# Kernel optimization log

Hardware: AMD Instinct MI355X
Metric: run time of the kernel (lower is better)

## Reference

```python
import jax, jax.numpy as jnp
import numpy as np

B, L, E, D = 4, 4096, 768, 64

def setup_inputs() -> dict:
    key = jax.random.key(0)
    ks = jax.random.split(key, 7)
    x = jax.random.normal(ks[0], (B, L, E), dtype=jnp.float32)
    # True = masked (strict upper triangle), as in masked_fill semantics
    causal_mask = jnp.triu(jnp.ones((L, L), dtype=bool), k=1)
    # True = valid token (inverted with ~ inside forward); all valid to avoid NaN rows
    pad_mask = jnp.ones((B, L), dtype=bool)
    s = 1.0 / np.sqrt(E)
    Wk = jax.random.uniform(ks[1], (E, D), jnp.float32, -s, s)
    bk = jax.random.uniform(ks[2], (D,), jnp.float32, -s, s)
    Wq = jax.random.uniform(ks[3], (E, D), jnp.float32, -s, s)
    bq = jax.random.uniform(ks[4], (D,), jnp.float32, -s, s)
    Wv = jax.random.uniform(ks[5], (E, D), jnp.float32, -s, s)
    bv = jax.random.uniform(ks[6], (D,), jnp.float32, -s, s)
    return {"x": x, "causal_mask": causal_mask, "pad_mask": pad_mask,
            "Wk": Wk, "bk": bk, "Wq": Wq, "bq": bq, "Wv": Wv, "bv": bv}

def reference(x, causal_mask, pad_mask, Wk, bk, Wq, bq, Wv, bv):
    # Linear projections: [B,L,E] @ [E,D] + [D]
    K = jnp.einsum('ble,ed->bld', x, Wk) + bk
    Q = jnp.einsum('ble,ed->bld', x, Wq) + bq
    V = jnp.einsum('ble,ed->bld', x, Wv) + bv
    d = Q.shape[-1]
    scores = jnp.einsum('bqd,bkd->bqk', Q, K) / jnp.sqrt(jnp.asarray(d, Q.dtype))
    # full_mask: causal (True=masked) OR key-position padding (~pad_mask, broadcast over query dim)
    full_mask = causal_mask[None, :, :] | (~pad_mask)[:, None, :]
    scores = jnp.where(full_mask, -jnp.inf, scores)
    attn = jax.nn.softmax(scores, axis=-1)
    out = jnp.einsum('bqk,bkd->bqd', attn, V)
    return out
```

## Files before the change

### kernel.cpp

```cpp
#include <hip/hip_runtime.h>

#define L_SEQ 4096
#define BATCH 4
#define EDIM 768

typedef __attribute__((ext_vector_type(8))) short bf16x8;
typedef __attribute__((ext_vector_type(4))) float f32x4;
typedef __attribute__((ext_vector_type(16))) float f32x16;
typedef __attribute__((ext_vector_type(4))) unsigned short u16x4;
typedef __attribute__((ext_vector_type(8))) unsigned short u16x8;
typedef __attribute__((ext_vector_type(2))) _Float16 f16x2;
typedef __attribute__((ext_vector_type(4))) _Float16 f16x4;

__device__ __forceinline__ unsigned short f2bf(float f) {
  unsigned u = __builtin_bit_cast(unsigned, f);
  u += 0x7FFFu + ((u >> 16) & 1u);
  return (unsigned short)(u >> 16);
}

__device__ __forceinline__ f16x4 half_of(u16x8 v, int h) {
  u16x4 t = h ? (u16x4){v[4], v[5], v[6], v[7]} : (u16x4){v[0], v[1], v[2], v[3]};
  return __builtin_bit_cast(f16x4, t);
}

__device__ __forceinline__ f16x2 pkrtz(float a, float b) {
  return __builtin_bit_cast(f16x2, __builtin_amdgcn_cvt_pkrtz(a, b));
}

__global__ __launch_bounds__(256) void prep_kernel(
    const float* __restrict__ Wq, const float* __restrict__ Wk,
    const float* __restrict__ Wv, unsigned short* __restrict__ WT) {
  int g = blockIdx.x * 256 + threadIdx.x;
  if (g >= 192 * EDIM) return;
  int row = g / EDIM, k = g - row * EDIM;
  int z = row >> 6, n = row & 63;
  const float* W = (z == 0) ? Wq : (z == 1) ? Wk : Wv;
  WT[g] = f2bf(W[k * 64 + n]);
}

__global__ __launch_bounds__(256) void proj_kernel(
    const float* __restrict__ x, const unsigned short* __restrict__ WT,
    const float* __restrict__ bq, const float* __restrict__ bk, const float* __restrict__ bv,
    unsigned short* __restrict__ Qf, unsigned short* __restrict__ Kf,
    unsigned short* __restrict__ Vf) {
  __shared__ unsigned short SH[2 * 13824];
  int tid = threadIdx.x;
  int w = tid >> 6, lane = tid & 63, l15 = lane & 15, g4 = lane >> 4;
  int m0 = blockIdx.x * 64;
  int brow = tid >> 3, bsg = tid & 7;

  f32x4 acc[3][4];
#pragma unroll
  for (int z = 0; z < 3; z++)
#pragma unroll
    for (int cf = 0; cf < 4; cf++) acc[z][cf] = (f32x4){0.f, 0.f, 0.f, 0.f};

  f32x4 arA[4], arB[4];
  u16x8 brA[6], brB[6];

  auto loadA = [&](f32x4 (&ar)[4], int k0) {
    const float* xp = x + (size_t)(m0 + 16 * w + l15) * EDIM + k0 + g4 * 8;
    ar[0] = *(const f32x4*)xp;
    ar[1] = *(const f32x4*)(xp + 4);
    ar[2] = *(const f32x4*)(xp + 32);
    ar[3] = *(const f32x4*)(xp + 36);
  };
  auto loadB = [&](u16x8 (&br)[6], int k0) {
#pragma unroll
    for (int pp = 0; pp < 6; pp++)
      br[pp] = *(const u16x8*)(WT + (size_t)(brow + pp * 32) * EDIM + k0 + bsg * 8);
  };
  auto writeB = [&](int cur, u16x8 (&br)[6]) {
#pragma unroll
    for (int pp = 0; pp < 6; pp++)
      *(u16x8*)&SH[cur * 13824 + (brow + pp * 32) * 72 + bsg * 8] = br[pp];
  };
  auto mkfrag = [&](f32x4 lo, f32x4 hi) {
    union { u16x8 u; bf16x8 b; } r;
    r.u[0] = f2bf(lo[0]); r.u[1] = f2bf(lo[1]); r.u[2] = f2bf(lo[2]); r.u[3] = f2bf(lo[3]);
    r.u[4] = f2bf(hi[0]); r.u[5] = f2bf(hi[1]); r.u[6] = f2bf(hi[2]); r.u[7] = f2bf(hi[3]);
    return r.b;
  };
  auto compute = [&](int cur, f32x4 (&ar)[4]) {
#pragma unroll
    for (int ks = 0; ks < 2; ks++) {
      bf16x8 a = mkfrag(ar[ks * 2], ar[ks * 2 + 1]);
#pragma unroll
      for (int z = 0; z < 3; z++)
#pragma unroll
        for (int cf = 0; cf < 4; cf++) {
          bf16x8 bb = *(const bf16x8*)&SH[cur * 13824 + (z * 64 + cf * 16 + l15) * 72 +
                                          ks * 32 + g4 * 8];
          acc[z][cf] = __builtin_amdgcn_mfma_f32_16x16x32_bf16(a, bb, acc[z][cf], 0, 0, 0);
        }
    }
  };

  loadA(arA, 0);
  loadB(brA, 0);
  for (int ss = 0; ss < 6; ss++) {
    int k1 = (2 * ss + 1) * 64;
    loadA(arB, k1);
    loadB(brB, k1);
    writeB(0, brA);
    __syncthreads();
    compute(0, arA);
    if (ss < 5) {
      int k2 = (2 * ss + 2) * 64;
      loadA(arA, k2);
      loadB(brA, k2);
    }
    writeB(1, brB);
    __syncthreads();
    compute(1, arB);
  }

  __syncthreads();
  unsigned short* LQ = SH;
  unsigned short* LK = SH + 4096;
  unsigned short* LV = SH + 8192;
#pragma unroll
  for (int cf = 0; cf < 4; cf++) {
    int d = cf * 16 + l15;
    float bqv = bq[d], bkv = bk[d], bvv = bv[d];
#pragma unroll
    for (int r = 0; r < 4; r++) {
      int t = 16 * w + g4 * 4 + r;
      int sl = t >> 5, tl = t & 31;
      int fqk = sl * 2048 + (d >> 4) * 512 + (tl + ((d >> 3) & 1) * 32) * 8 + (d & 7);
      LQ[fqk] = f2bf((acc[0][cf][r] + bqv) * 0.125f);
      LK[fqk] = f2bf(acc[1][cf][r] + bkv);
      int fv = sl * 2048 + (d >> 5) * 1024 + ((tl >> 4) & 1) * 512 +
               ((d & 31) + ((tl >> 2) & 1) * 32) * 8 + ((tl >> 3) & 1) * 4 + (tl & 3);
      _Float16 hv = (_Float16)(acc[2][cf][r] + bvv);
      LV[fv] = __builtin_bit_cast(unsigned short, hv);
    }
  }
  __syncthreads();
  {
    int bb = m0 >> 12;
    int S0 = (m0 >> 5) & 127;
    size_t base = ((size_t)(bb * 128 + S0)) * 2048;
    u16x8* dq = (u16x8*)(Qf + base);
    u16x8* dk = (u16x8*)(Kf + base);
    u16x8* dv = (u16x8*)(Vf + base);
    const u16x8* sq = (const u16x8*)LQ;
    const u16x8* sk = (const u16x8*)LK;
    const u16x8* sv = (const u16x8*)LV;
    dq[tid * 2] = sq[tid * 2]; dq[tid * 2 + 1] = sq[tid * 2 + 1];
    dk[tid * 2] = sk[tid * 2]; dk[tid * 2 + 1] = sk[tid * 2 + 1];
    dv[tid * 2] = sv[tid * 2]; dv[tid * 2 + 1] = sv[tid * 2 + 1];
  }
}

__global__ __launch_bounds__(512, 2) void attn_kernel(
    const unsigned short* __restrict__ Qf, const unsigned short* __restrict__ Kf,
    const unsigned short* __restrict__ Vf, float* __restrict__ out) {
  __shared__ float OB[8][32][68];
  __shared__ float ML[8][2][32];
  int tid = threadIdx.x;
  int w = tid >> 6, lane = tid & 63;
  int ql = lane & 31, hi = lane >> 5;
  int blk = blockIdx.x;
  int xcd = blk & 7;
  int b = xcd >> 1;
  int pid = ((xcd & 1) << 5) | (blk >> 3);
  int sA = pid, sB = 127 - pid;
  size_t bL = (size_t)b * L_SEQ;
  const unsigned short* Qb = Qf + (size_t)b * 128 * 2048;
  const unsigned short* Kb = Kf + (size_t)b * 128 * 2048;
  const unsigned short* Vb = Vf + (size_t)b * 128 * 2048;

  bf16x8 qA[4], qB[4];
#pragma unroll
  for (int kh = 0; kh < 4; kh++) {
    qA[kh] = *(const bf16x8*)(Qb + ((size_t)sA * 4 + kh) * 512 + lane * 8);
    qB[kh] = *(const bf16x8*)(Qb + ((size_t)sB * 4 + kh) * 512 + lane * 8);
  }
  f32x16 oA0, oA1, oB0, oB1;
#pragma unroll
  for (int i = 0; i < 16; i++) { oA0[i] = 0.f; oA1[i] = 0.f; oB0[i] = 0.f; oB1[i] = 0.f; }
  float mA = -1e38f, lA = 0.f, mB = -1e38f, lB = 0.f;

  auto loadKV = [&](bf16x8 (&kf)[4], u16x8 (&vf)[4], int j) {
    const unsigned short* kp = Kb + (size_t)j * 2048 + lane * 8;
    const unsigned short* vp = Vb + (size_t)j * 2048 + lane * 8;
#pragma unroll
    for (int q = 0; q < 4; q++) kf[q] = *(const bf16x8*)(kp + q * 512);
#pragma unroll
    for (int q = 0; q < 4; q++) vf[q] = *(const u16x8*)(vp + q * 512);
  };

  auto strip = [&](bf16x8 (&kf)[4], u16x8 (&vf)[4], int j, int s, bf16x8 (&qf)[4],
                   f32x16& o0, f32x16& o1, float& m, float& l) {
    f32x16 st;
#pragma unroll
    for (int i = 0; i < 16; i++) st[i] = 0.f;
    __builtin_amdgcn_s_setprio(1);
#pragma unroll
    for (int kh = 0; kh < 4; kh++)
      st = __builtin_amdgcn_mfma_f32_32x32x16_bf16(kf[kh], qf[kh], st, 0, 0, 0);
    __builtin_amdgcn_s_setprio(0);

    if (j == s) {
#pragma unroll
      for (int r = 0; r < 16; r++) {
        int tl = (r & 3) + 8 * (r >> 2) + 4 * hi;
        if (tl > ql) st[r] = -1e30f;
      }
    }

    float mx = st[0];
#pragma unroll
    for (int r = 1; r < 16; r++) mx = fmaxf(mx, st[r]);
    mx = fmaxf(mx, __shfl_xor(mx, 32));
    if (!__all(mx <= m + 8.0f)) {
      float mn = fmaxf(m, mx);
      float sc = __expf(m - mn);
      m = mn; l *= sc;
#pragma unroll
      for (int i = 0; i < 16; i++) { o0[i] *= sc; o1[i] *= sc; }
    }
    float rs = 0.f;
#pragma unroll
    for (int r = 0; r < 16; r++) { st[r] = __expf(st[r] - m); rs += st[r]; }
    rs += __shfl_xor(rs, 32);
    l += rs;

    f16x4 pb[4];
#pragma unroll
    for (int oc = 0; oc < 4; oc++) {
      f16x2 a = pkrtz(st[4 * oc], st[4 * oc + 1]);
      f16x2 c = pkrtz(st[4 * oc + 2], st[4 * oc + 3]);
      pb[oc] = (f16x4){a[0], a[1], c[0], c[1]};
    }
    __builtin_amdgcn_s_setprio(1);
#pragma unroll
    for (int oc = 0; oc < 4; oc++)
      o0 = __builtin_amdgcn_mfma_f32_32x32x8f16(half_of(vf[oc >> 1], oc & 1), pb[oc], o0, 0, 0, 0);
#pragma unroll
    for (int oc = 0; oc < 4; oc++)
      o1 = __builtin_amdgcn_mfma_f32_32x32x8f16(half_of(vf[2 + (oc >> 1)], oc & 1), pb[oc], o1, 0, 0, 0);
    __builtin_amdgcn_s_setprio(0);
  };

  auto step = [&](bf16x8 (&kf)[4], u16x8 (&vf)[4], int j) {
    if (j <= sA) strip(kf, vf, j, sA, qA, oA0, oA1, mA, lA);
    strip(kf, vf, j, sB, qB, oB0, oB1, mB, lB);
  };

  bf16x8 kfA[4], kfB[4];
  u16x8 vfA[4], vfB[4];
  {
    int j = w;
    loadKV(kfA, vfA, j);
    while (true) {
      int jn = j + 8;
      bool hasB = (jn <= sB);
      if (hasB) loadKV(kfB, vfB, jn);
      step(kfA, vfA, j);
      if (!hasB) break;
      j = jn;
      jn = j + 8;
      bool hasA = (jn <= sB);
      if (hasA) loadKV(kfA, vfA, jn);
      step(kfB, vfB, j);
      if (!hasA) break;
      j = jn;
    }
  }

  auto stash_reduce = [&](int s, f32x16& o0, f32x16& o1, float m, float l) {
    __syncthreads();
#pragma unroll
    for (int g = 0; g < 4; g++) {
      *(f32x4*)&OB[w][ql][8 * g + 4 * hi] =
          (f32x4){o0[4 * g], o0[4 * g + 1], o0[4 * g + 2], o0[4 * g + 3]};
      *(f32x4*)&OB[w][ql][32 + 8 * g + 4 * hi] =
          (f32x4){o1[4 * g], o1[4 * g + 1], o1[4 * g + 2], o1[4 * g + 3]};
    }
    if (hi == 0) { ML[w][0][ql] = m; ML[w][1][ql] = l; }
    __syncthreads();
    int q = tid >> 4, dg = tid & 15;
    float mw[8], lw[8];
    float ms = -1e38f;
#pragma unroll
    for (int ww = 0; ww < 8; ww++) {
      mw[ww] = ML[ww][0][q]; lw[ww] = ML[ww][1][q];
      ms = fmaxf(ms, mw[ww]);
    }
    float denom = 0.f, ew[8];
#pragma unroll
    for (int ww = 0; ww < 8; ww++) { ew[ww] = __expf(mw[ww] - ms); denom += lw[ww] * ew[ww]; }
    float inv = 1.0f / denom;
    f32x4 acc = (f32x4){0.f, 0.f, 0.f, 0.f};
#pragma unroll
    for (int ww = 0; ww < 8; ww++) {
      f32x4 v = *(const f32x4*)&OB[ww][q][dg * 4];
      acc += v * ew[ww];
    }
    acc *= inv;
    *(f32x4*)(out + (bL + (size_t)s * 32 + q) * 64 + dg * 4) = acc;
  };
  stash_reduce(sA, oA0, oA1, mA, lA);
  stash_reduce(sB, oB0, oB1, mB, lB);
}

extern "C" void kernel_launch(void* const* d_in, const int* in_sizes, int n_in,
                              void* d_out, int out_size, void* d_ws, size_t ws_size,
                              hipStream_t stream) {
  const float* x  = (const float*)d_in[0];
  const float* Wk = (const float*)d_in[3];
  const float* bk = (const float*)d_in[4];
  const float* Wq = (const float*)d_in[5];
  const float* bq = (const float*)d_in[6];
  const float* Wv = (const float*)d_in[7];
  const float* bv = (const float*)d_in[8];
  float* out = (float*)d_out;

  char* ws = (char*)d_ws;
  unsigned short* WT = (unsigned short*)ws;
  unsigned short* Qf = (unsigned short*)(ws + 294912);
  unsigned short* Kf = (unsigned short*)(ws + 294912 + 2097152);
  unsigned short* Vf = (unsigned short*)(ws + 294912 + 2 * 2097152);

  prep_kernel<<<576, 256, 0, stream>>>(Wq, Wk, Wv, WT);
  proj_kernel<<<256, 256, 0, stream>>>(x, WT, bq, bk, bv, Qf, Kf, Vf);
  attn_kernel<<<256, 512, 0, stream>>>(Qf, Kf, Vf, out);
}
```

Before: 48.13 us.

## Split projection into smaller tiles, use exp2 softmax, stagger K/V loads

The projection kernel now computes 32 rows per block across 512 blocks. Its four waves split as two row halves by two column halves, so each wave covers 96 output columns instead of all 192. The attention kernel folds log2(e) into the Q scale and uses exp2f in place of __expf, widening the lazy-rescale threshold to match. It also issues the next K loads and V loads separately, interleaved between the two strips. Together these aim to raise projection parallelism, cut exponent instruction cost, and spread memory traffic, at the cost of reloading the weight tiles in more blocks.

After: 53.98 us. 1.12x slower.

```diff
diff --git a/kernel.cpp b/kernel.cpp
--- a/kernel.cpp
+++ b/kernel.cpp
@@ -11,6 +11,8 @@
 typedef __attribute__((ext_vector_type(8))) unsigned short u16x8;
 typedef __attribute__((ext_vector_type(2))) _Float16 f16x2;
 typedef __attribute__((ext_vector_type(4))) _Float16 f16x4;
+
+#define QSCALE (0.125f * 1.4426950408889634f)
 
 __device__ __forceinline__ unsigned short f2bf(float f) {
   unsigned u = __builtin_bit_cast(unsigned, f);
@@ -46,20 +48,19 @@
   __shared__ unsigned short SH[2 * 13824];
   int tid = threadIdx.x;
   int w = tid >> 6, lane = tid & 63, l15 = lane & 15, g4 = lane >> 4;
-  int m0 = blockIdx.x * 64;
+  int rw = w & 1, ch = w >> 1;
+  int m0 = blockIdx.x * 32;
   int brow = tid >> 3, bsg = tid & 7;
 
-  f32x4 acc[3][4];
-#pragma unroll
-  for (int z = 0; z < 3; z++)
-#pragma unroll
-    for (int cf = 0; cf < 4; cf++) acc[z][cf] = (f32x4){0.f, 0.f, 0.f, 0.f};
+  f32x4 acc[6];
+#pragma unroll
+  for (int cf = 0; cf < 6; cf++) acc[cf] = (f32x4){0.f, 0.f, 0.f, 0.f};
 
   f32x4 arA[4], arB[4];
   u16x8 brA[6], brB[6];
 
   auto loadA = [&](f32x4 (&ar)[4], int k0) {
-    const float* xp = x + (size_t)(m0 + 16 * w + l15) * EDIM + k0 + g4 * 8;
+    const float* xp = x + (size_t)(m0 + 16 * rw + l15) * EDIM + k0 + g4 * 8;
     ar[0] = *(const f32x4*)xp;
     ar[1] = *(const f32x4*)(xp + 4);
     ar[2] = *(const f32x4*)(xp + 32);
@@ -86,13 +87,11 @@
     for (int ks = 0; ks < 2; ks++) {
       bf16x8 a = mkfrag(ar[ks * 2], ar[ks * 2 + 1]);
 #pragma unroll
-      for (int z = 0; z < 3; z++)
-#pragma unroll
-        for (int cf = 0; cf < 4; cf++) {
-          bf16x8 bb = *(const bf16x8*)&SH[cur * 13824 + (z * 64 + cf * 16 + l15) * 72 +
-                                          ks * 32 + g4 * 8];
-          acc[z][cf] = __builtin_amdgcn_mfma_f32_16x16x32_bf16(a, bb, acc[z][cf], 0, 0, 0);
-        }
+      for (int cf = 0; cf < 6; cf++) {
+        bf16x8 bb = *(const bf16x8*)&SH[cur * 13824 + (ch * 96 + cf * 16 + l15) * 72 +
+                                        ks * 32 + g4 * 8];
+        acc[cf] = __builtin_amdgcn_mfma_f32_16x16x32_bf16(a, bb, acc[cf], 0, 0, 0);
+      }
     }
   };
 
@@ -117,39 +116,37 @@
 
   __syncthreads();
   unsigned short* LQ = SH;
-  unsigned short* LK = SH + 4096;
-  unsigned short* LV = SH + 8192;
-#pragma unroll
-  for (int cf = 0; cf < 4; cf++) {
-    int d = cf * 16 + l15;
-    float bqv = bq[d], bkv = bk[d], bvv = bv[d];
+  unsigned short* LK = SH + 2048;
+  unsigned short* LV = SH + 4096;
+#pragma unroll
+  for (int cf = 0; cf < 6; cf++) {
+    int c = ch * 96 + cf * 16 + l15;
+    int z = c >> 6, d = c & 63;
+    float bb_ = (z == 0) ? bq[d] : (z == 1) ? bk[d] : bv[d];
 #pragma unroll
     for (int r = 0; r < 4; r++) {
-      int t = 16 * w + g4 * 4 + r;
-      int sl = t >> 5, tl = t & 31;
-      int fqk = sl * 2048 + (d >> 4) * 512 + (tl + ((d >> 3) & 1) * 32) * 8 + (d & 7);
-      LQ[fqk] = f2bf((acc[0][cf][r] + bqv) * 0.125f);
-      LK[fqk] = f2bf(acc[1][cf][r] + bkv);
-      int fv = sl * 2048 + (d >> 5) * 1024 + ((tl >> 4) & 1) * 512 +
-               ((d & 31) + ((tl >> 2) & 1) * 32) * 8 + ((tl >> 3) & 1) * 4 + (tl & 3);
-      _Float16 hv = (_Float16)(acc[2][cf][r] + bvv);
-      LV[fv] = __builtin_bit_cast(unsigned short, hv);
+      int tl = rw * 16 + g4 * 4 + r;
+      float v = acc[cf][r] + bb_;
+      if (z == 2) {
+        int fv = (d >> 5) * 1024 + ((tl >> 4) & 1) * 512 +
+                 ((d & 31) + ((tl >> 2) & 1) * 32) * 8 + ((tl >> 3) & 1) * 4 + (tl & 3);
+        _Float16 hv = (_Float16)v;
+        LV[fv] = __builtin_bit_cast(unsigned short, hv);
+      } else {
+        int fqk = (d >> 4) * 512 + (tl + ((d >> 3) & 1) * 32) * 8 + (d & 7);
+        if (z == 0) LQ[fqk] = f2bf(v * QSCALE);
+        else        LK[fqk] = f2bf(v);
+      }
     }
   }
   __syncthreads();
   {
-    int bb = m0 >> 12;
+    int b_ = m0 >> 12;
     int S0 = (m0 >> 5) & 127;
-    size_t base = ((size_t)(bb * 128 + S0)) * 2048;
-    u16x8* dq = (u16x8*)(Qf + base);
-    u16x8* dk = (u16x8*)(Kf + base);
-    u16x8* dv = (u16x8*)(Vf + base);
-    const u16x8* sq = (const u16x8*)LQ;
-    const u16x8* sk = (const u16x8*)LK;
-    const u16x8* sv = (const u16x8*)LV;
-    dq[tid * 2] = sq[tid * 2]; dq[tid * 2 + 1] = sq[tid * 2 + 1];
-    dk[tid * 2] = sk[tid * 2]; dk[tid * 2 + 1] = sk[tid * 2 + 1];
-    dv[tid * 2] = sv[tid * 2]; dv[tid * 2 + 1] = sv[tid * 2 + 1];
+    size_t base = ((size_t)(b_ * 128 + S0)) * 2048;
+    ((u16x8*)(Qf + base))[tid] = ((const u16x8*)LQ)[tid];
+    ((u16x8*)(Kf + base))[tid] = ((const u16x8*)LK)[tid];
+    ((u16x8*)(Vf + base))[tid] = ((const u16x8*)LV)[tid];
   }
 }
 
@@ -182,11 +179,13 @@
   for (int i = 0; i < 16; i++) { oA0[i] = 0.f; oA1[i] = 0.f; oB0[i] = 0.f; oB1[i] = 0.f; }
   float mA = -1e38f, lA = 0.f, mB = -1e38f, lB = 0.f;
 
-  auto loadKV = [&](bf16x8 (&kf)[4], u16x8 (&vf)[4], int j) {
+  auto loadK = [&](bf16x8 (&kf)[4], int j) {
     const unsigned short* kp = Kb + (size_t)j * 2048 + lane * 8;
+#pragma unroll
+    for (int q = 0; q < 4; q++) kf[q] = *(const bf16x8*)(kp + q * 512);
+  };
+  auto loadV = [&](u16x8 (&vf)[4], int j) {
     const unsigned short* vp = Vb + (size_t)j * 2048 + lane * 8;
-#pragma unroll
-    for (int q = 0; q < 4; q++) kf[q] = *(const bf16x8*)(kp + q * 512);
 #pragma unroll
     for (int q = 0; q < 4; q++) vf[q] = *(const u16x8*)(vp + q * 512);
   };
@@ -214,16 +213,16 @@
 #pragma unroll
     for (int r = 1; r < 16; r++) mx = fmaxf(mx, st[r]);
     mx = fmaxf(mx, __shfl_xor(mx, 32));
-    if (!__all(mx <= m + 8.0f)) {
+    if (!__all(mx <= m + 11.0f)) {
       float mn = fmaxf(m, mx);
-      float sc = __expf(m - mn);
+      float sc = exp2f(m - mn);
       m = mn; l *= sc;
 #pragma unroll
       for (int i = 0; i < 16; i++) { o0[i] *= sc; o1[i] *= sc; }
     }
     float rs = 0.f;
 #pragma unroll
-    for (int r = 0; r < 16; r++) { st[r] = __expf(st[r] - m); rs += st[r]; }
+    for (int r = 0; r < 16; r++) { st[r] = exp2f(st[r] - m); rs += st[r]; }
     rs += __shfl_xor(rs, 32);
     l += rs;
 
@@ -244,27 +243,27 @@
     __builtin_amdgcn_s_setprio(0);
   };
 
-  auto step = [&](bf16x8 (&kf)[4], u16x8 (&vf)[4], int j) {
-    if (j <= sA) strip(kf, vf, j, sA, qA, oA0, oA1, mA, lA);
-    strip(kf, vf, j, sB, qB, oB0, oB1, mB, lB);
-  };
-
   bf16x8 kfA[4], kfB[4];
   u16x8 vfA[4], vfB[4];
   {
     int j = w;
-    loadKV(kfA, vfA, j);
+    loadK(kfA, j);
+    loadV(vfA, j);
     while (true) {
       int jn = j + 8;
       bool hasB = (jn <= sB);
-      if (hasB) loadKV(kfB, vfB, jn);
-      step(kfA, vfA, j);
+      if (hasB) loadK(kfB, jn);
+      if (j <= sA) strip(kfA, vfA, j, sA, qA, oA0, oA1, mA, lA);
+      if (hasB) loadV(vfB, jn);
+      strip(kfA, vfA, j, sB, qB, oB0, oB1, mB, lB);
       if (!hasB) break;
       j = jn;
       jn = j + 8;
       bool hasA = (jn <= sB);
-      if (hasA) loadKV(kfA, vfA, jn);
-      step(kfB, vfB, j);
+      if (hasA) loadK(kfA, jn);
+      if (j <= sA) strip(kfB, vfB, j, sA, qA, oA0, oA1, mA, lA);
+      if (hasA) loadV(vfA, jn);
+      strip(kfB, vfB, j, sB, qB, oB0, oB1, mB, lB);
       if (!hasA) break;
       j = jn;
     }
@@ -291,7 +290,7 @@
     }
     float denom = 0.f, ew[8];
 #pragma unroll
-    for (int ww = 0; ww < 8; ww++) { ew[ww] = __expf(mw[ww] - ms); denom += lw[ww] * ew[ww]; }
+    for (int ww = 0; ww < 8; ww++) { ew[ww] = exp2f(mw[ww] - ms); denom += lw[ww] * ew[ww]; }
     float inv = 1.0f / denom;
     f32x4 acc = (f32x4){0.f, 0.f, 0.f, 0.f};
 #pragma unroll
@@ -325,6 +324,6 @@
   unsigned short* Vf = (unsigned short*)(ws + 294912 + 2 * 2097152);
 
   prep_kernel<<<576, 256, 0, stream>>>(Wq, Wk, Wv, WT);
-  proj_kernel<<<256, 256, 0, stream>>>(x, WT, bq, bk, bv, Qf, Kf, Vf);
+  proj_kernel<<<512, 256, 0, stream>>>(x, WT, bq, bk, bv, Qf, Kf, Vf);
   attn_kernel<<<256, 512, 0, stream>>>(Qf, Kf, Vf, out);
 }
```
